# Performance work log

Measured on AMD Instinct MI355X. Metric: run time of the kernel, lower is better.

Reference implementation:

```python
import jax, jax.numpy as jnp
import numpy as np

N = 100000   # nodes
E = 1600000  # edges (avg degree 16)
D = 128      # input_dim = hidden_dim = output_dim


def setup_inputs() -> dict:
    key = jax.random.key(0)
    ks = jax.random.split(key, 16)
    s = 0.02
    inp = {
        "node_emb": jax.random.normal(ks[0], (N, D), dtype=jnp.float32),
        "edge_index": jax.random.randint(ks[1], (2, E), 0, N, dtype=jnp.int64),
        # last-layer GCN branch (conv1 -> relu -> conv2); earlier layers are dead code in SSL.forward
        "gcn_w1": jax.random.normal(ks[2], (D, D), dtype=jnp.float32) * s,
        "gcn_b1": jnp.zeros((D,), dtype=jnp.float32),
        "gcn_w2": jax.random.normal(ks[3], (D, D), dtype=jnp.float32) * s,
        "gcn_b2": jnp.zeros((D,), dtype=jnp.float32),
        # last-layer GIN branch (GINConv eps=0, Mlp == single Linear)
        "gin_w1": jax.random.normal(ks[4], (D, D), dtype=jnp.float32) * s,
        "gin_b1": jnp.zeros((D,), dtype=jnp.float32),
        "gin_w2": jax.random.normal(ks[5], (D, D), dtype=jnp.float32) * s,
        "gin_b2": jnp.zeros((D,), dtype=jnp.float32),
        # fusion heads
        "lin_w": jax.random.normal(ks[6], (D, D), dtype=jnp.float32) * s,
        "lin_b": jnp.zeros((D,), dtype=jnp.float32),
        "fc_w": jax.random.normal(ks[7], (D, D), dtype=jnp.float32) * s,
        "fc_b": jnp.zeros((D,), dtype=jnp.float32),
    }
    return inp


def reference(node_emb, edge_index, gcn_w1, gcn_b1, gcn_w2, gcn_b2,
              gin_w1, gin_b1, gin_w2, gin_b2, lin_w, lin_b, fc_w, fc_b):
    n = node_emb.shape[0]
    src, dst = edge_index[0], edge_index[1]

    # symmetric GCN normalization with self-loops: deg counts incoming edges + 1
    deg = jax.ops.segment_sum(jnp.ones(src.shape[0], node_emb.dtype), dst, num_segments=n) + 1.0
    dinv = jax.lax.rsqrt(deg)                  # deg >= 1 always
    edge_norm = dinv[src] * dinv[dst]          # [E]
    self_norm = dinv * dinv                    # [N] self-loop coefficient

    def gcn_conv(x, W, b):
        y = x @ W                                                        # [N, D]
        agg = jax.ops.segment_sum(y[src] * edge_norm[:, None], dst, num_segments=n)
        return agg + self_norm[:, None] * y + b

    def gin_conv(x, W, b):
        # GINConv(train_eps=False): nn((1+0)*x + sum_{j in N(i)} x_j), nn = Linear
        agg = jax.ops.segment_sum(x[src], dst, num_segments=n)
        return (x + agg) @ W + b

    # GCN branch: conv1 -> relu -> (dropout=identity in eval) -> conv2
    h = jax.nn.relu(gcn_conv(node_emb, gcn_w1, gcn_b1))
    x_gcn = gcn_conv(h, gcn_w2, gcn_b2)

    # GIN branch: conv1 -> conv2
    g = gin_conv(node_emb, gin_w1, gin_b1)
    x_gin = gin_conv(g, gin_w2, gin_b2)

    # fusion heads
    x_gin = x_gin @ lin_w + lin_b
    x_gcn = x_gcn @ lin_w + lin_b
    return (x_gin + x_gcn) @ fc_w + fc_b
```

## Files before the change

kernel.cpp:

```cpp
#include <hip/hip_runtime.h>

#define D 128
#define HS_LD 136

using s8v = __attribute__((ext_vector_type(8))) short;
using f4v = __attribute__((ext_vector_type(4))) float;

__device__ __forceinline__ float bf2f(ushort u) {
  union { uint i; float f; } v; v.i = ((uint)u) << 16; return v.f;
}
__device__ __forceinline__ ushort f2bf(float f) {
  union { float f; uint i; } v; v.f = f;
  uint b = v.i;
  return (ushort)((b + 0x7fffu + ((b >> 16) & 1u)) >> 16);
}

__global__ void megaA_kernel(const int* __restrict__ dst, int* __restrict__ ideg,
                             int* __restrict__ pos, int E,
                             const float* __restrict__ x, ushort* __restrict__ xb, long total,
                             const float* __restrict__ lw, const float* __restrict__ fw,
                             float* __restrict__ LF,
                             const float* __restrict__ gw1, ushort* __restrict__ T1g) {
  int b = blockIdx.x;
  if (b < 2048) {
    int i = b * 256 + threadIdx.x;
    int stride = 2048 * 256;
    for (int e = i; e < E; e += stride)
      pos[e] = atomicAdd(&ideg[dst[e]], 1);
  } else if (b < 5248) {
    long i = ((long)(b - 2048) * 256 + threadIdx.x) * 8;
    long stride = (long)3200 * 256 * 8;
    for (long t = i; t < total; t += stride) {
      float4 v0 = *(const float4*)(x + t);
      float4 v1 = *(const float4*)(x + t + 4);
      s8v u;
      u[0] = (short)f2bf(v0.x); u[1] = (short)f2bf(v0.y);
      u[2] = (short)f2bf(v0.z); u[3] = (short)f2bf(v0.w);
      u[4] = (short)f2bf(v1.x); u[5] = (short)f2bf(v1.y);
      u[6] = (short)f2bf(v1.z); u[7] = (short)f2bf(v1.w);
      *(s8v*)(xb + t) = u;
    }
  } else if (b < 5312) {
    int t = (b - 5248) * 256 + threadIdx.x;
    int r = t >> 7, c = t & 127;
    float s = 0.f;
#pragma unroll 8
    for (int k = 0; k < 128; ++k) s = fmaf(lw[r * 128 + k], fw[k * 128 + c], s);
    LF[r * 128 + c] = s;
  } else {
    int t = (b - 5312) * 256 + threadIdx.x;
    int k = t >> 7, c = t & 127;
    T1g[c * 128 + k] = f2bf(gw1[k * 128 + c]);
  }
}

__global__ void scanP_kernel(const int* __restrict__ deg, int* __restrict__ incl,
                             int* __restrict__ bsum, int n, int nb,
                             const float* __restrict__ iw2, const float* __restrict__ gw2,
                             const float* __restrict__ LF,
                             float* __restrict__ M2i, ushort* __restrict__ W2gT,
                             const float* __restrict__ gb2, const float* __restrict__ ib2,
                             const float* __restrict__ lb, const float* __restrict__ fw,
                             const float* __restrict__ fb, float* __restrict__ btot) {
  int b = blockIdx.x;
  if (b < nb) {
    __shared__ int tmp[256];
    int t = threadIdx.x;
    int i = b * 256 + t;
    int v = (i < n) ? deg[i] : 0;
    tmp[t] = v;
    __syncthreads();
#pragma unroll
    for (int off = 1; off < 256; off <<= 1) {
      int u = (t >= off) ? tmp[t - off] : 0;
      __syncthreads();
      tmp[t] += u;
      __syncthreads();
    }
    if (i < n) incl[i] = tmp[t];
    if (t == 255) bsum[b] = tmp[255];
  } else if (b < nb + 64) {
    int t = (b - nb) * 256 + threadIdx.x;
    int k = t >> 7, c = t & 127;
    float s = 0.f;
#pragma unroll 8
    for (int j = 0; j < 128; ++j) s = fmaf(iw2[k * 128 + j], LF[j * 128 + c], s);
    M2i[k * 128 + c] = s;
  } else if (b < nb + 128) {
    int t = (b - nb - 64) * 256 + threadIdx.x;
    int k = t >> 7, c = t & 127;
    float s = 0.f;
#pragma unroll 8
    for (int j = 0; j < 128; ++j) s = fmaf(gw2[k * 128 + j], LF[j * 128 + c], s);
    W2gT[c * 128 + k] = f2bf(s);
  } else if (threadIdx.x < 128) {
    int c = threadIdx.x;
    float s = fb[c];
#pragma unroll 8
    for (int j = 0; j < 128; ++j) {
      s = fmaf(gb2[j] + ib2[j], LF[j * 128 + c], s);
      s = fmaf(2.f * lb[j], fw[j * 128 + c], s);
    }
    btot[c] = s;
  }
}

__global__ void scan2F_kernel(int* __restrict__ bsum, int nb,
                              const float* __restrict__ iw1, const float* __restrict__ M2i,
                              ushort* __restrict__ WginT,
                              const float* __restrict__ ib1, float* __restrict__ bgin) {
  int b = blockIdx.x;
  if (b == 0) {
    __shared__ int tmp[256];
    __shared__ int carry_s;
    int t = threadIdx.x;
    if (t == 0) carry_s = 0;
    __syncthreads();
    for (int base = 0; base < nb; base += 256) {
      int v = (base + t < nb) ? bsum[base + t] : 0;
      tmp[t] = v;
      __syncthreads();
#pragma unroll
      for (int off = 1; off < 256; off <<= 1) {
        int u = (t >= off) ? tmp[t - off] : 0;
        __syncthreads();
        tmp[t] += u;
        __syncthreads();
      }
      int inc = tmp[t] + carry_s;
      if (base + t < nb) bsum[base + t] = inc;
      __syncthreads();
      if (t == 255) carry_s = inc;
      __syncthreads();
    }
  } else if (b <= 64) {
    int t = (b - 1) * 256 + threadIdx.x;
    int k = t >> 7, c = t & 127;
    float s = 0.f;
#pragma unroll 8
    for (int j = 0; j < 128; ++j) s = fmaf(iw1[k * 128 + j], M2i[j * 128 + c], s);
    WginT[c * 128 + k] = f2bf(s);
  } else if (threadIdx.x < 128) {
    int c = threadIdx.x;
    float s = 0.f;
#pragma unroll 8
    for (int j = 0; j < 128; ++j) s = fmaf(ib1[j], M2i[j * 128 + c], s);
    bgin[c] = s;
  }
}

__global__ void scan3_kernel(const int* __restrict__ deg, const int* __restrict__ incl,
                             const int* __restrict__ bsum, int* __restrict__ rowptr,
                             float* __restrict__ dinv, int n, int E) {
  int i = blockIdx.x * 256 + threadIdx.x;
  if (i < n) {
    int carry = (blockIdx.x > 0) ? bsum[blockIdx.x - 1] : 0;
    int d = deg[i];
    rowptr[i] = incl[i] - d + carry;
    dinv[i] = rsqrtf((float)d + 1.0f);
  }
  if (i == 0) rowptr[n] = E;
}

__global__ void scatter_kernel(const int* __restrict__ src, const int* __restrict__ dst,
                               const int* __restrict__ rowptr, const int* __restrict__ pos,
                               int* __restrict__ csrc, int E) {
  int i = blockIdx.x * blockDim.x + threadIdx.x;
  int stride = gridDim.x * blockDim.x;
  for (int e = i; e < E; e += stride)
    csrc[rowptr[dst[e]] + pos[e]] = src[e];
}

__global__ __launch_bounds__(256) void gatherA_kernel(
    const ushort* __restrict__ xb, const float* __restrict__ dinv,
    const int* __restrict__ rowptr, const int* __restrict__ csrc,
    ushort* __restrict__ ab, int n) {
  int nd = blockIdx.x * 4 + (threadIdx.x >> 6);
  if (nd >= n) return;
  int lane = threadIdx.x & 63;
  int half = lane >> 5;
  int hl = lane & 31;
  int beg = rowptr[nd], end = rowptr[nd + 1];
  ushort4 us = *(const ushort4*)(xb + (long)nd * D + 4 * hl);
  float dd = dinv[nd];
  float4 sg = make_float4(0.f, 0.f, 0.f, 0.f);
  float4 sc = make_float4(0.f, 0.f, 0.f, 0.f);
  int j = beg + half;
  for (; j + 6 < end; j += 8) {
    int s0 = csrc[j], s1 = csrc[j + 2], s2 = csrc[j + 4], s3 = csrc[j + 6];
    float w0 = dinv[s0], w1 = dinv[s1], w2 = dinv[s2], w3 = dinv[s3];
    ushort4 v0 = *(const ushort4*)(xb + (long)s0 * D + 4 * hl);
    ushort4 v1 = *(const ushort4*)(xb + (long)s1 * D + 4 * hl);
    ushort4 v2 = *(const ushort4*)(xb + (long)s2 * D + 4 * hl);
    ushort4 v3 = *(const ushort4*)(xb + (long)s3 * D + 4 * hl);
    float a0 = bf2f(v0.x), a1 = bf2f(v0.y), a2 = bf2f(v0.z), a3 = bf2f(v0.w);
    sg.x += a0; sg.y += a1; sg.z += a2; sg.w += a3;
    sc.x = fmaf(w0, a0, sc.x); sc.y = fmaf(w0, a1, sc.y);
    sc.z = fmaf(w0, a2, sc.z); sc.w = fmaf(w0, a3, sc.w);
    a0 = bf2f(v1.x); a1 = bf2f(v1.y); a2 = bf2f(v1.z); a3 = bf2f(v1.w);
    sg.x += a0; sg.y += a1; sg.z += a2; sg.w += a3;
    sc.x = fmaf(w1, a0, sc.x); sc.y = fmaf(w1, a1, sc.y);
    sc.z = fmaf(w1, a2, sc.z); sc.w = fmaf(w1, a3, sc.w);
    a0 = bf2f(v2.x); a1 = bf2f(v2.y); a2 = bf2f(v2.z); a3 = bf2f(v2.w);
    sg.x += a0; sg.y += a1; sg.z += a2; sg.w += a3;
    sc.x = fmaf(w2, a0, sc.x); sc.y = fmaf(w2, a1, sc.y);
    sc.z = fmaf(w2, a2, sc.z); sc.w = fmaf(w2, a3, sc.w);
    a0 = bf2f(v3.x); a1 = bf2f(v3.y); a2 = bf2f(v3.z); a3 = bf2f(v3.w);
    sg.x += a0; sg.y += a1; sg.z += a2; sg.w += a3;
    sc.x = fmaf(w3, a0, sc.x); sc.y = fmaf(w3, a1, sc.y);
    sc.z = fmaf(w3, a2, sc.z); sc.w = fmaf(w3, a3, sc.w);
  }
  if (j + 2 < end) {
    int s0 = csrc[j], s1 = csrc[j + 2];
    float w0 = dinv[s0], w1 = dinv[s1];
    ushort4 v0 = *(const ushort4*)(xb + (long)s0 * D + 4 * hl);
    ushort4 v1 = *(const ushort4*)(xb + (long)s1 * D + 4 * hl);
    float a0 = bf2f(v0.x), a1 = bf2f(v0.y), a2 = bf2f(v0.z), a3 = bf2f(v0.w);
    sg.x += a0; sg.y += a1; sg.z += a2; sg.w += a3;
    sc.x = fmaf(w0, a0, sc.x); sc.y = fmaf(w0, a1, sc.y);
    sc.z = fmaf(w0, a2, sc.z); sc.w = fmaf(w0, a3, sc.w);
    a0 = bf2f(v1.x); a1 = bf2f(v1.y); a2 = bf2f(v1.z); a3 = bf2f(v1.w);
    sg.x += a0; sg.y += a1; sg.z += a2; sg.w += a3;
    sc.x = fmaf(w1, a0, sc.x); sc.y = fmaf(w1, a1, sc.y);
    sc.z = fmaf(w1, a2, sc.z); sc.w = fmaf(w1, a3, sc.w);
    j += 4;
  }
  for (; j < end; j += 2) {
    int s0 = csrc[j];
    float w0 = dinv[s0];
    ushort4 v0 = *(const ushort4*)(xb + (long)s0 * D + 4 * hl);
    float a0 = bf2f(v0.x), a1 = bf2f(v0.y), a2 = bf2f(v0.z), a3 = bf2f(v0.w);
    sg.x += a0; sg.y += a1; sg.z += a2; sg.w += a3;
    sc.x = fmaf(w0, a0, sc.x); sc.y = fmaf(w0, a1, sc.y);
    sc.z = fmaf(w0, a2, sc.z); sc.w = fmaf(w0, a3, sc.w);
  }
  sg.x += __shfl_xor(sg.x, 32); sg.y += __shfl_xor(sg.y, 32);
  sg.z += __shfl_xor(sg.z, 32); sg.w += __shfl_xor(sg.w, 32);
  sc.x += __shfl_xor(sc.x, 32); sc.y += __shfl_xor(sc.y, 32);
  sc.z += __shfl_xor(sc.z, 32); sc.w += __shfl_xor(sc.w, 32);

  float x0 = bf2f(us.x), x1 = bf2f(us.y), x2 = bf2f(us.z), x3 = bf2f(us.w);
  ushort4 o;
  if (half == 0) {
    o.x = f2bf(dd * (sc.x + dd * x0));
    o.y = f2bf(dd * (sc.y + dd * x1));
    o.z = f2bf(dd * (sc.z + dd * x2));
    o.w = f2bf(dd * (sc.w + dd * x3));
    *(ushort4*)(ab + (long)nd * 256 + 4 * hl) = o;
  } else {
    o.x = f2bf(x0 + sg.x);
    o.y = f2bf(x1 + sg.y);
    o.z = f2bf(x2 + sg.z);
    o.w = f2bf(x3 + sg.w);
    *(ushort4*)(ab + (long)nd * 256 + 128 + 4 * hl) = o;
  }
}

__global__ __launch_bounds__(256) void gemm1_kernel(
    const ushort* __restrict__ ab,
    const ushort* __restrict__ T1g, const ushort* __restrict__ WginT,
    const ushort* __restrict__ W2gT,
    const float* __restrict__ gb1, const float* __restrict__ bgin,
    const float* __restrict__ dinv,
    ushort* __restrict__ pq, int n) {
  __shared__ ushort Ws[128 * 128];
  __shared__ ushort Hs[128 * HS_LD];
  const int y = blockIdx.y;
  const int tid = threadIdx.x;
  const int wave = tid >> 6, lane = tid & 63;
  const int rlo = lane & 15, khi = lane >> 4;
  const int rb = blockIdx.x * 128 + wave * 32;

  s8v a[2][4];
#pragma unroll
  for (int rt = 0; rt < 2; ++rt) {
    int row = rb + rt * 16 + rlo;
    row = row < n ? row : n - 1;
    const ushort* p = ab + (long)row * 256 + y * 128 + khi * 8;
#pragma unroll
    for (int ks = 0; ks < 4; ++ks) a[rt][ks] = *(const s8v*)(p + ks * 32);
  }

  {
    const ushort* W = y ? WginT : T1g;
#pragma unroll
    for (int j = 0; j < 8; ++j) {
      int q = tid + 256 * j;
      int c = q >> 4, kc = q & 15;
      *(s8v*)&Ws[c * 128 + ((kc ^ (c & 7)) << 3)] = *(const s8v*)(W + c * 128 + kc * 8);
    }
  }
  __syncthreads();

  f4v acc[2][8];
#pragma unroll
  for (int rt = 0; rt < 2; ++rt)
#pragma unroll
    for (int ct = 0; ct < 8; ++ct) acc[rt][ct] = (f4v){0.f, 0.f, 0.f, 0.f};

#pragma unroll
  for (int ks = 0; ks < 4; ++ks) {
#pragma unroll
    for (int ct = 0; ct < 8; ++ct) {
      int c = ct * 16 + rlo;
      int kc = ks * 4 + khi;
      s8v b = *(const s8v*)&Ws[c * 128 + ((kc ^ (c & 7)) << 3)];
      acc[0][ct] = __builtin_amdgcn_mfma_f32_16x16x32_bf16(a[0][ks], b, acc[0][ct], 0, 0, 0);
      acc[1][ct] = __builtin_amdgcn_mfma_f32_16x16x32_bf16(a[1][ks], b, acc[1][ct], 0, 0, 0);
    }
  }

  if (y == 1) {
#pragma unroll
    for (int ct = 0; ct < 8; ++ct) {
      int col = ct * 16 + rlo;
      float bb = bgin[col];
#pragma unroll
      for (int rt = 0; rt < 2; ++rt) {
#pragma unroll
        for (int i = 0; i < 4; ++i) {
          int row = rb + rt * 16 + 4 * khi + i;
          if (row < n)
            pq[(long)row * 256 + 128 + col] = f2bf(acc[rt][ct][i] + bb);
        }
      }
    }
    return;
  }

  __syncthreads();
#pragma unroll
  for (int ct = 0; ct < 8; ++ct) {
    int col = ct * 16 + rlo;
    float bb = gb1[col];
#pragma unroll
    for (int rt = 0; rt < 2; ++rt) {
#pragma unroll
      for (int i = 0; i < 4; ++i) {
        int r = wave * 32 + rt * 16 + 4 * khi + i;
        Hs[r * HS_LD + col] = f2bf(fmaxf(acc[rt][ct][i] + bb, 0.f));
      }
    }
  }
#pragma unroll
  for (int j = 0; j < 8; ++j) {
    int q = tid + 256 * j;
    int c = q >> 4, kc = q & 15;
    *(s8v*)&Ws[c * 128 + ((kc ^ (c & 7)) << 3)] = *(const s8v*)(W2gT + c * 128 + kc * 8);
  }
  __syncthreads();

  s8v a2[2][4];
#pragma unroll
  for (int rt = 0; rt < 2; ++rt) {
    int r = wave * 32 + rt * 16 + rlo;
#pragma unroll
    for (int ks = 0; ks < 4; ++ks)
      a2[rt][ks] = *(const s8v*)&Hs[r * HS_LD + (ks * 4 + khi) * 8];
  }

  f4v acc2[2][8];
#pragma unroll
  for (int rt = 0; rt < 2; ++rt)
#pragma unroll
    for (int ct = 0; ct < 8; ++ct) acc2[rt][ct] = (f4v){0.f, 0.f, 0.f, 0.f};

#pragma unroll
  for (int ks = 0; ks < 4; ++ks) {
#pragma unroll
    for (int ct = 0; ct < 8; ++ct) {
      int c = ct * 16 + rlo;
      int kc = ks * 4 + khi;
      s8v b = *(const s8v*)&Ws[c * 128 + ((kc ^ (c & 7)) << 3)];
      acc2[0][ct] = __builtin_amdgcn_mfma_f32_16x16x32_bf16(a2[0][ks], b, acc2[0][ct], 0, 0, 0);
      acc2[1][ct] = __builtin_amdgcn_mfma_f32_16x16x32_bf16(a2[1][ks], b, acc2[1][ct], 0, 0, 0);
    }
  }

  float ddv[2][4];
#pragma unroll
  for (int rt = 0; rt < 2; ++rt)
#pragma unroll
    for (int i = 0; i < 4; ++i) {
      int row = rb + rt * 16 + 4 * khi + i;
      ddv[rt][i] = (row < n) ? dinv[row] : 0.f;
    }

#pragma unroll
  for (int ct = 0; ct < 8; ++ct) {
    int col = ct * 16 + rlo;
#pragma unroll
    for (int rt = 0; rt < 2; ++rt) {
#pragma unroll
      for (int i = 0; i < 4; ++i) {
        int row = rb + rt * 16 + 4 * khi + i;
        if (row < n)
          pq[(long)row * 256 + col] = f2bf(ddv[rt][i] * acc2[rt][ct][i]);
      }
    }
  }
}

__global__ __launch_bounds__(256) void gatherB_kernel(
    const ushort* __restrict__ pq, const float* __restrict__ dinv,
    const int* __restrict__ rowptr, const int* __restrict__ csrc,
    const float* __restrict__ btot, float* __restrict__ out, int n) {
  int nd = blockIdx.x * 4 + (threadIdx.x >> 6);
  if (nd >= n) return;
  int lane = threadIdx.x & 63;
  int half = lane >> 5;
  int hl = lane & 31;
  int beg = rowptr[nd], end = rowptr[nd + 1];
  ushort4 u = *(const ushort4*)(pq + (long)nd * 256 + lane * 4);
  float dd = dinv[nd];
  float4 s = make_float4(0.f, 0.f, 0.f, 0.f);
  int j = beg;
  for (; j + 7 < end; j += 8) {
    int s0 = csrc[j],     s1 = csrc[j + 1], s2 = csrc[j + 2], s3 = csrc[j + 3];
    int s4 = csrc[j + 4], s5 = csrc[j + 5], s6 = csrc[j + 6], s7 = csrc[j + 7];
    ushort4 v0 = *(const ushort4*)(pq + (long)s0 * 256 + lane * 4);
    ushort4 v1 = *(const ushort4*)(pq + (long)s1 * 256 + lane * 4);
    ushort4 v2 = *(const ushort4*)(pq + (long)s2 * 256 + lane * 4);
    ushort4 v3 = *(const ushort4*)(pq + (long)s3 * 256 + lane * 4);
    ushort4 v4 = *(const ushort4*)(pq + (long)s4 * 256 + lane * 4);
    ushort4 v5 = *(const ushort4*)(pq + (long)s5 * 256 + lane * 4);
    ushort4 v6 = *(const ushort4*)(pq + (long)s6 * 256 + lane * 4);
    ushort4 v7 = *(const ushort4*)(pq + (long)s7 * 256 + lane * 4);
    s.x += ((bf2f(v0.x) + bf2f(v1.x)) + (bf2f(v2.x) + bf2f(v3.x))) +
           ((bf2f(v4.x) + bf2f(v5.x)) + (bf2f(v6.x) + bf2f(v7.x)));
    s.y += ((bf2f(v0.y) + bf2f(v1.y)) + (bf2f(v2.y) + bf2f(v3.y))) +
           ((bf2f(v4.y) + bf2f(v5.y)) + (bf2f(v6.y) + bf2f(v7.y)));
    s.z += ((bf2f(v0.z) + bf2f(v1.z)) + (bf2f(v2.z) + bf2f(v3.z))) +
           ((bf2f(v4.z) + bf2f(v5.z)) + (bf2f(v6.z) + bf2f(v7.z)));
    s.w += ((bf2f(v0.w) + bf2f(v1.w)) + (bf2f(v2.w) + bf2f(v3.w))) +
           ((bf2f(v4.w) + bf2f(v5.w)) + (bf2f(v6.w) + bf2f(v7.w)));
  }
  if (j + 1 < end) {
    int s0 = csrc[j], s1 = csrc[j + 1];
    ushort4 v0 = *(const ushort4*)(pq + (long)s0 * 256 + lane * 4);
    ushort4 v1 = *(const ushort4*)(pq + (long)s1 * 256 + lane * 4);
    s.x += bf2f(v0.x) + bf2f(v1.x);
    s.y += bf2f(v0.y) + bf2f(v1.y);
    s.z += bf2f(v0.z) + bf2f(v1.z);
    s.w += bf2f(v0.w) + bf2f(v1.w);
    j += 2;
    if (j + 1 < end) {
      int s2 = csrc[j], s3 = csrc[j + 1];
      ushort4 v2 = *(const ushort4*)(pq + (long)s2 * 256 + lane * 4);
      ushort4 v3 = *(const ushort4*)(pq + (long)s3 * 256 + lane * 4);
      s.x += bf2f(v2.x) + bf2f(v3.x);
      s.y += bf2f(v2.y) + bf2f(v3.y);
      s.z += bf2f(v2.z) + bf2f(v3.z);
      s.w += bf2f(v2.w) + bf2f(v3.w);
      j += 2;
      if (j + 1 < end) {
        int s4 = csrc[j], s5 = csrc[j + 1];
        ushort4 v4 = *(const ushort4*)(pq + (long)s4 * 256 + lane * 4);
        ushort4 v5 = *(const ushort4*)(pq + (long)s5 * 256 + lane * 4);
        s.x += bf2f(v4.x) + bf2f(v5.x);
        s.y += bf2f(v4.y) + bf2f(v5.y);
        s.z += bf2f(v4.z) + bf2f(v5.z);
        s.w += bf2f(v4.w) + bf2f(v5.w);
        j += 2;
      }
    }
  }
  if (j < end) {
    int s0 = csrc[j];
    ushort4 v0 = *(const ushort4*)(pq + (long)s0 * 256 + lane * 4);
    s.x += bf2f(v0.x); s.y += bf2f(v0.y);
    s.z += bf2f(v0.z); s.w += bf2f(v0.w);
  }
  float4 o;
  if (half == 0) {
    o.x = dd * (s.x + bf2f(u.x));
    o.y = dd * (s.y + bf2f(u.y));
    o.z = dd * (s.z + bf2f(u.z));
    o.w = dd * (s.w + bf2f(u.w));
  } else {
    o.x = s.x + bf2f(u.x);
    o.y = s.y + bf2f(u.y);
    o.z = s.z + bf2f(u.z);
    o.w = s.w + bf2f(u.w);
  }
  o.x += __shfl_xor(o.x, 32);
  o.y += __shfl_xor(o.y, 32);
  o.z += __shfl_xor(o.z, 32);
  o.w += __shfl_xor(o.w, 32);
  if (half == 0) {
    float4 bt = *(const float4*)(btot + 4 * hl);
    o.x += bt.x; o.y += bt.y; o.z += bt.z; o.w += bt.w;
    *(float4*)(out + (long)nd * D + 4 * hl) = o;
  }
}

extern "C" void kernel_launch(void* const* d_in, const int* in_sizes, int n_in,
                              void* d_out, int out_size, void* d_ws, size_t ws_size,
                              hipStream_t stream) {
  const float* x   = (const float*)d_in[0];
  const int*   ei  = (const int*)d_in[1];
  const float* gw1 = (const float*)d_in[2];
  const float* gb1 = (const float*)d_in[3];
  const float* gw2 = (const float*)d_in[4];
  const float* gb2 = (const float*)d_in[5];
  const float* iw1 = (const float*)d_in[6];
  const float* ib1 = (const float*)d_in[7];
  const float* iw2 = (const float*)d_in[8];
  const float* ib2 = (const float*)d_in[9];
  const float* lw  = (const float*)d_in[10];
  const float* lb  = (const float*)d_in[11];
  const float* fw  = (const float*)d_in[12];
  const float* fb  = (const float*)d_in[13];
  float* out = (float*)d_out;

  const int n = in_sizes[0] / D;
  const int E = in_sizes[1] / 2;
  const int* src = ei;
  const int* dst = ei + E;
  const int nb = (n + 255) / 256;
  const long ND = (long)n * D;

  char* p = (char*)d_ws;
  auto alloc = [&](size_t bytes) {
    char* r = p;
    p += (bytes + 255) & ~(size_t)255;
    return r;
  };
  int* ideg    = (int*)alloc((size_t)n * 4);
  int* incl    = (int*)alloc((size_t)n * 4);
  int* rowptr  = (int*)alloc((size_t)(n + 1) * 4);
  int* bsum    = (int*)alloc(1024 * 4);
  int* pos     = (int*)alloc((size_t)E * 4);
  int* csrc    = (int*)alloc((size_t)E * 4);
  float* dinv  = (float*)alloc((size_t)n * 4);
  float* LF    = (float*)alloc(16384 * 4);
  float* M2i   = (float*)alloc(16384 * 4);
  float* btot  = (float*)alloc(128 * 4);
  float* bgin  = (float*)alloc(128 * 4);
  ushort* xb   = (ushort*)alloc(ND * 2);
  ushort* T1g   = (ushort*)alloc(16384 * 2);
  ushort* WginT = (ushort*)alloc(16384 * 2);
  ushort* W2gT  = (ushort*)alloc(16384 * 2);
  ushort* ab   = (ushort*)alloc(2 * ND * 2);
  ushort* pq   = (ushort*)alloc(2 * ND * 2);

  hipMemsetAsync(ideg, 0, (size_t)n * 4, stream);

  megaA_kernel<<<5376, 256, 0, stream>>>(dst, ideg, pos, E, x, xb, ND, lw, fw, LF, gw1, T1g);
  scanP_kernel<<<nb + 129, 256, 0, stream>>>(ideg, incl, bsum, n, nb, iw2, gw2, LF,
                                             M2i, W2gT, gb2, ib2, lb, fw, fb, btot);
  scan2F_kernel<<<66, 256, 0, stream>>>(bsum, nb, iw1, M2i, WginT, ib1, bgin);
  scan3_kernel<<<nb, 256, 0, stream>>>(ideg, incl, bsum, rowptr, dinv, n, E);
  scatter_kernel<<<2048, 256, 0, stream>>>(src, dst, rowptr, pos, csrc, E);

  gatherA_kernel<<<(n + 3) / 4, 256, 0, stream>>>(xb, dinv, rowptr, csrc, ab, n);
  const int nblk = (n + 127) / 128;
  gemm1_kernel<<<dim3(nblk, 2), 256, 0, stream>>>(ab, T1g, WginT, W2gT, gb1, bgin, dinv, pq, n);
  gatherB_kernel<<<(n + 3) / 4, 256, 0, stream>>>(pq, dinv, rowptr, csrc, btot, out, n);
}
```

Baseline: 377.6 us.

## Merge three scan kernels into single-pass decoupled look-back scan

Replaces the three-kernel prefix scan (block scan, carry scan, fixup) with one kernel that uses a decoupled look-back over per-block status words, writing rowptr and dinv directly. The weight-folding matmuls (M2i then WginT and bgin) are also fused into the same launch, with each block computing one M2i column in shared memory and reusing it, so the M2i buffer and two launches go away. The memset is widened to also zero the status array. It also drops a partial unroll stage in gatherA and moves the self-row load after the neighbour loop. The look-back spin relies on earlier blocks being scheduled first, which adds a forward-progress risk.

```diff
diff --git a/kernel.cpp b/kernel.cpp
--- a/kernel.cpp
+++ b/kernel.cpp
@@ -54,18 +54,24 @@
   }
 }
 
-__global__ void scanP_kernel(const int* __restrict__ deg, int* __restrict__ incl,
-                             int* __restrict__ bsum, int n, int nb,
-                             const float* __restrict__ iw2, const float* __restrict__ gw2,
-                             const float* __restrict__ LF,
-                             float* __restrict__ M2i, ushort* __restrict__ W2gT,
+__global__ void scanF_kernel(const int* __restrict__ deg,
+                             unsigned long long* __restrict__ partial,
+                             int* __restrict__ rowptr, float* __restrict__ dinv,
+                             int n, int nbScan, int E,
+                             const float* __restrict__ gw2, const float* __restrict__ iw1,
+                             const float* __restrict__ iw2, const float* __restrict__ LF,
+                             ushort* __restrict__ W2gT, ushort* __restrict__ WginT,
+                             const float* __restrict__ ib1, float* __restrict__ bgin,
                              const float* __restrict__ gb2, const float* __restrict__ ib2,
                              const float* __restrict__ lb, const float* __restrict__ fw,
-                             const float* __restrict__ fb, float* __restrict__ btot) {
-  int b = blockIdx.x;
-  if (b < nb) {
-    __shared__ int tmp[256];
-    int t = threadIdx.x;
+                             const float* __restrict__ fcb, float* __restrict__ btot) {
+  __shared__ int tmp[256];
+  __shared__ int prefix_s;
+  __shared__ float m2col[128];
+  const int b = blockIdx.x;
+  const int t = threadIdx.x;
+
+  if (b < nbScan) {
     int i = b * 256 + t;
     int v = (i < n) ? deg[i] : 0;
     tmp[t] = v;
@@ -77,25 +83,66 @@
       tmp[t] += u;
       __syncthreads();
     }
-    if (i < n) incl[i] = tmp[t];
-    if (t == 255) bsum[b] = tmp[255];
-  } else if (b < nb + 64) {
-    int t = (b - nb) * 256 + threadIdx.x;
-    int k = t >> 7, c = t & 127;
-    float s = 0.f;
-#pragma unroll 8
-    for (int j = 0; j < 128; ++j) s = fmaf(iw2[k * 128 + j], LF[j * 128 + c], s);
-    M2i[k * 128 + c] = s;
-  } else if (b < nb + 128) {
-    int t = (b - nb - 64) * 256 + threadIdx.x;
-    int k = t >> 7, c = t & 127;
+    int T = tmp[255];
+    if (t == 0) {
+      unsigned long long st = ((b == 0 ? 2ull : 1ull) << 62) | (unsigned long long)(unsigned)T;
+      atomicExch(&partial[b], st);
+      long long acc = 0;
+      if (b > 0) {
+        int k = b - 1;
+        while (true) {
+          unsigned long long pv = atomicAdd(&partial[k], 0ull);
+          unsigned long long s2 = pv >> 62;
+          if (s2 == 0) continue;
+          acc += (long long)(pv & 0xFFFFFFFFull);
+          if (s2 == 2ull) break;
+          --k;
+        }
+        atomicExch(&partial[b], (2ull << 62) | (unsigned long long)(unsigned)(acc + T));
+      }
+      prefix_s = (int)acc;
+    }
+    __syncthreads();
+    int prefix = prefix_s;
+    if (i < n) {
+      rowptr[i] = prefix + tmp[t] - v;
+      dinv[i] = rsqrtf((float)v + 1.0f);
+    }
+    if (i == 0) rowptr[n] = E;
+    return;
+  }
+
+  int wb = b - nbScan;
+  if (wb < 64) {
+    int q = wb * 256 + t;
+    int k = q >> 7, c = q & 127;
     float s = 0.f;
 #pragma unroll 8
     for (int j = 0; j < 128; ++j) s = fmaf(gw2[k * 128 + j], LF[j * 128 + c], s);
     W2gT[c * 128 + k] = f2bf(s);
-  } else if (threadIdx.x < 128) {
-    int c = threadIdx.x;
-    float s = fb[c];
+  } else if (wb < 192) {
+    int c = wb - 64;
+    if (t < 128) {
+      float s = 0.f;
+#pragma unroll 8
+      for (int m = 0; m < 128; ++m) s = fmaf(iw2[t * 128 + m], LF[m * 128 + c], s);
+      m2col[t] = s;
+    }
+    __syncthreads();
+    if (t < 128) {
+      float s = 0.f;
+#pragma unroll 8
+      for (int j = 0; j < 128; ++j) s = fmaf(iw1[t * 128 + j], m2col[j], s);
+      WginT[c * 128 + t] = f2bf(s);
+    } else if (t == 128) {
+      float s = 0.f;
+#pragma unroll 8
+      for (int j = 0; j < 128; ++j) s = fmaf(ib1[j], m2col[j], s);
+      bgin[c] = s;
+    }
+  } else if (t < 128) {
+    int c = t;
+    float s = fcb[c];
 #pragma unroll 8
     for (int j = 0; j < 128; ++j) {
       s = fmaf(gb2[j] + ib2[j], LF[j * 128 + c], s);
@@ -103,63 +150,6 @@
     }
     btot[c] = s;
   }
-}
-
-__global__ void scan2F_kernel(int* __restrict__ bsum, int nb,
-                              const float* __restrict__ iw1, const float* __restrict__ M2i,
-                              ushort* __restrict__ WginT,
-                              const float* __restrict__ ib1, float* __restrict__ bgin) {
-  int b = blockIdx.x;
-  if (b == 0) {
-    __shared__ int tmp[256];
-    __shared__ int carry_s;
-    int t = threadIdx.x;
-    if (t == 0) carry_s = 0;
-    __syncthreads();
-    for (int base = 0; base < nb; base += 256) {
-      int v = (base + t < nb) ? bsum[base + t] : 0;
-      tmp[t] = v;
-      __syncthreads();
-#pragma unroll
-      for (int off = 1; off < 256; off <<= 1) {
-        int u = (t >= off) ? tmp[t - off] : 0;
-        __syncthreads();
-        tmp[t] += u;
-        __syncthreads();
-      }
-      int inc = tmp[t] + carry_s;
-      if (base + t < nb) bsum[base + t] = inc;
-      __syncthreads();
-      if (t == 255) carry_s = inc;
-      __syncthreads();
-    }
-  } else if (b <= 64) {
-    int t = (b - 1) * 256 + threadIdx.x;
-    int k = t >> 7, c = t & 127;
-    float s = 0.f;
-#pragma unroll 8
-    for (int j = 0; j < 128; ++j) s = fmaf(iw1[k * 128 + j], M2i[j * 128 + c], s);
-    WginT[c * 128 + k] = f2bf(s);
-  } else if (threadIdx.x < 128) {
-    int c = threadIdx.x;
-    float s = 0.f;
-#pragma unroll 8
-    for (int j = 0; j < 128; ++j) s = fmaf(ib1[j], M2i[j * 128 + c], s);
-    bgin[c] = s;
-  }
-}
-
-__global__ void scan3_kernel(const int* __restrict__ deg, const int* __restrict__ incl,
-                             const int* __restrict__ bsum, int* __restrict__ rowptr,
-                             float* __restrict__ dinv, int n, int E) {
-  int i = blockIdx.x * 256 + threadIdx.x;
-  if (i < n) {
-    int carry = (blockIdx.x > 0) ? bsum[blockIdx.x - 1] : 0;
-    int d = deg[i];
-    rowptr[i] = incl[i] - d + carry;
-    dinv[i] = rsqrtf((float)d + 1.0f);
-  }
-  if (i == 0) rowptr[n] = E;
 }
 
 __global__ void scatter_kernel(const int* __restrict__ src, const int* __restrict__ dst,
@@ -181,8 +171,6 @@
   int half = lane >> 5;
   int hl = lane & 31;
   int beg = rowptr[nd], end = rowptr[nd + 1];
-  ushort4 us = *(const ushort4*)(xb + (long)nd * D + 4 * hl);
-  float dd = dinv[nd];
   float4 sg = make_float4(0.f, 0.f, 0.f, 0.f);
   float4 sc = make_float4(0.f, 0.f, 0.f, 0.f);
   int j = beg + half;
@@ -210,21 +198,6 @@
     sc.x = fmaf(w3, a0, sc.x); sc.y = fmaf(w3, a1, sc.y);
     sc.z = fmaf(w3, a2, sc.z); sc.w = fmaf(w3, a3, sc.w);
   }
-  if (j + 2 < end) {
-    int s0 = csrc[j], s1 = csrc[j + 2];
-    float w0 = dinv[s0], w1 = dinv[s1];
-    ushort4 v0 = *(const ushort4*)(xb + (long)s0 * D + 4 * hl);
-    ushort4 v1 = *(const ushort4*)(xb + (long)s1 * D + 4 * hl);
-    float a0 = bf2f(v0.x), a1 = bf2f(v0.y), a2 = bf2f(v0.z), a3 = bf2f(v0.w);
-    sg.x += a0; sg.y += a1; sg.z += a2; sg.w += a3;
-    sc.x = fmaf(w0, a0, sc.x); sc.y = fmaf(w0, a1, sc.y);
-    sc.z = fmaf(w0, a2, sc.z); sc.w = fmaf(w0, a3, sc.w);
-    a0 = bf2f(v1.x); a1 = bf2f(v1.y); a2 = bf2f(v1.z); a3 = bf2f(v1.w);
-    sg.x += a0; sg.y += a1; sg.z += a2; sg.w += a3;
-    sc.x = fmaf(w1, a0, sc.x); sc.y = fmaf(w1, a1, sc.y);
-    sc.z = fmaf(w1, a2, sc.z); sc.w = fmaf(w1, a3, sc.w);
-    j += 4;
-  }
   for (; j < end; j += 2) {
     int s0 = csrc[j];
     float w0 = dinv[s0];
@@ -239,7 +212,9 @@
   sc.x += __shfl_xor(sc.x, 32); sc.y += __shfl_xor(sc.y, 32);
   sc.z += __shfl_xor(sc.z, 32); sc.w += __shfl_xor(sc.w, 32);
 
+  ushort4 us = *(const ushort4*)(xb + (long)nd * D + 4 * hl);
   float x0 = bf2f(us.x), x1 = bf2f(us.y), x2 = bf2f(us.z), x3 = bf2f(us.w);
+  float dd = dinv[nd];
   ushort4 o;
   if (half == 0) {
     o.x = f2bf(dd * (sc.x + dd * x0));
@@ -527,14 +502,12 @@
     return r;
   };
   int* ideg    = (int*)alloc((size_t)n * 4);
-  int* incl    = (int*)alloc((size_t)n * 4);
+  unsigned long long* partial = (unsigned long long*)alloc((size_t)nb * 8);
   int* rowptr  = (int*)alloc((size_t)(n + 1) * 4);
-  int* bsum    = (int*)alloc(1024 * 4);
   int* pos     = (int*)alloc((size_t)E * 4);
   int* csrc    = (int*)alloc((size_t)E * 4);
   float* dinv  = (float*)alloc((size_t)n * 4);
   float* LF    = (float*)alloc(16384 * 4);
-  float* M2i   = (float*)alloc(16384 * 4);
   float* btot  = (float*)alloc(128 * 4);
   float* bgin  = (float*)alloc(128 * 4);
   ushort* xb   = (ushort*)alloc(ND * 2);
@@ -544,13 +517,13 @@
   ushort* ab   = (ushort*)alloc(2 * ND * 2);
   ushort* pq   = (ushort*)alloc(2 * ND * 2);
 
-  hipMemsetAsync(ideg, 0, (size_t)n * 4, stream);
+  size_t idegPad = ((size_t)n * 4 + 255) & ~(size_t)255;
+  (void)hipMemsetAsync(ideg, 0, idegPad + (size_t)nb * 8, stream);
 
   megaA_kernel<<<5376, 256, 0, stream>>>(dst, ideg, pos, E, x, xb, ND, lw, fw, LF, gw1, T1g);
-  scanP_kernel<<<nb + 129, 256, 0, stream>>>(ideg, incl, bsum, n, nb, iw2, gw2, LF,
-                                             M2i, W2gT, gb2, ib2, lb, fw, fb, btot);
-  scan2F_kernel<<<66, 256, 0, stream>>>(bsum, nb, iw1, M2i, WginT, ib1, bgin);
-  scan3_kernel<<<nb, 256, 0, stream>>>(ideg, incl, bsum, rowptr, dinv, n, E);
+  scanF_kernel<<<nb + 193, 256, 0, stream>>>(ideg, partial, rowptr, dinv, n, nb, E,
+                                             gw2, iw1, iw2, LF, W2gT, WginT,
+                                             ib1, bgin, gb2, ib2, lb, fw, fb, btot);
   scatter_kernel<<<2048, 256, 0, stream>>>(src, dst, rowptr, pos, csrc, E);
 
   gatherA_kernel<<<(n + 3) / 4, 256, 0, stream>>>(xb, dinv, rowptr, csrc, ab, n);
```

Result: no change. 375.7 us (-0.5%).
